# Kernel optimization log

Measured on AMD Instinct MI355X. Metric: run time of the kernel, lower is better.

## Reference

```python
import jax, jax.numpy as jnp
import numpy as np

BS, N, NP, K = 2, 4096, 1024, 8   # batch, fine pts, coarse pts, in-degree per fine node
CI, CO, MID = 32, 16, 32          # in channels (16 skip + 16 interpolated), out channels, radial MLP width
E = BS * N * K


def setup_inputs() -> dict:
    key = jax.random.key(0)
    ks = iter(jax.random.split(key, 64))
    nrm = lambda s, sc=1.0: jax.random.normal(next(ks), s, jnp.float32) * sc
    inp = {}
    inp['h0'] = nrm((BS * N, 16, 1))
    inp['h1'] = nrm((BS * N, 16, 3))
    inp['uph0'] = nrm((BS * NP, 16, 1))
    inp['uph1'] = nrm((BS * NP, 16, 3))
    inp['xyz'] = jax.random.uniform(next(ks), (BS, N, 3), jnp.float32)
    inp['xyz_prev'] = jax.random.uniform(next(ks), (BS, NP, 3), jnp.float32)
    dst = jnp.repeat(jnp.arange(BS * N, dtype=jnp.int32), K)
    src = (dst // N) * N + jax.random.randint(next(ks), (E,), 0, N, jnp.int32)
    inp['edge_src'], inp['edge_dst'] = src, dst
    xf = inp['xyz'].reshape(BS * N, 3)
    inp['r'] = jnp.linalg.norm(xf[src] - xf[dst], axis=-1, keepdims=True)
    # CG basis tensors basis[din,dout]: [E, 2*dout+1, 2*din+1, 2*min(din,dout)+1]
    inp['basis00'] = nrm((E, 1, 1, 1))
    inp['basis01'] = nrm((E, 3, 1, 1))
    inp['basis10'] = nrm((E, 1, 3, 1))
    inp['basis11'] = nrm((E, 3, 3, 3))
    for p, f in (('00', 1), ('01', 1), ('10', 1), ('11', 3)):
        inp['rw1_' + p] = nrm((1, MID), 0.5)
        inp['rb1_' + p] = jnp.zeros((MID,), jnp.float32)
        inp['rw2_' + p] = nrm((MID, MID), 0.2)
        inp['rb2_' + p] = jnp.zeros((MID,), jnp.float32)
        inp['rw3_' + p] = nrm((MID, CO * CI * f), 0.1)
    inp['wself0'] = nrm((CO, CI), 0.1)
    inp['wself1'] = nrm((CO, CI), 0.1)
    inp['gamma0'] = jnp.ones((CO,), jnp.float32)
    inp['beta0'] = jnp.zeros((CO,), jnp.float32)
    inp['gamma1'] = jnp.ones((CO,), jnp.float32)
    inp['beta1'] = jnp.zeros((CO,), jnp.float32)
    return inp


def _radial(r, w1, b1, w2, b2, w3, f):
    x = jax.nn.relu(r @ w1 + b1)
    x = jax.nn.relu(x @ w2 + b2)
    return (x @ w3).reshape(E, CO, CI, f)


def _pair_msg(basis, hsrc, R):
    # basis [E,mo,mi,f], hsrc [E,ci,mi], R [E,co,ci,f] -> msg [E,co,mo]
    # (fused form of per-edge kernel = sum_f R*basis followed by kernel @ src)
    tmp = jnp.einsum('emnf,ein->eimf', basis, hsrc)
    return jnp.einsum('eoif,eimf->eom', R, tmp)


def _gnorm(h, gamma, beta):
    # GNormSE3: norm over m-dim, LayerNorm+ReLU on norms, rescale phase
    n = jnp.sqrt(jnp.sum(h * h, -1) + 1e-12)           # [Nn,co]
    phase = h / n[..., None]
    mu = jnp.mean(n, -1, keepdims=True)
    var = jnp.var(n, -1, keepdims=True)
    t = jax.nn.relu((n - mu) / jnp.sqrt(var + 1e-5) * gamma + beta)
    return t[..., None] * phase


def _fwd(h0, h1, uph0, uph1, xyz, xyz_prev, r, basis00, basis01, basis10, basis11,
         rw1_00, rb1_00, rw2_00, rb2_00, rw3_00,
         rw1_01, rb1_01, rw2_01, rb2_01, rw3_01,
         rw1_10, rb1_10, rw2_10, rb2_10, rw3_10,
         rw1_11, rb1_11, rw2_11, rb2_11, rw3_11,
         wself0, wself1, gamma0, beta0, gamma1, beta1, edge_src, edge_dst):
    # --- three_nn + inverse-squared-distance interpolation of coarse features ---
    d2 = jnp.sum((xyz[:, :, None, :] - xyz_prev[:, None, :, :]) ** 2, -1)  # [B,N,NP]
    negd, idx = jax.lax.top_k(-d2, 3)
    dist = jnp.sqrt(jnp.maximum(-negd, 0.0))
    d2c = jnp.maximum(dist * dist, 1e-10)
    inv = 1.0 / (d2c + 1e-8)
    w = inv / jnp.sum(inv, -1, keepdims=True)          # [B,N,3]

    def interp(uph):
        C, F = uph.shape[1], uph.shape[2]
        fp = uph.reshape(BS, NP, C * F)
        g = jax.vmap(lambda f_, i_: f_[i_])(fp, idx)   # [B,N,3,C*F]
        return jnp.sum(g * w[..., None], 2).reshape(BS * N, C, F)

    h0c = jnp.concatenate([interp(uph0), h0], 1)       # [BN,CI,1]
    h1c = jnp.concatenate([interp(uph1), h1], 1)       # [BN,CI,3]

    # --- GConvSE3: per-edge CG-basis kernels, mean aggregation, self-interaction ---
    hs0, hs1 = h0c[edge_src], h1c[edge_src]
    R00 = _radial(r, rw1_00, rb1_00, rw2_00, rb2_00, rw3_00, 1)
    R01 = _radial(r, rw1_01, rb1_01, rw2_01, rb2_01, rw3_01, 1)
    R10 = _radial(r, rw1_10, rb1_10, rw2_10, rb2_10, rw3_10, 1)
    R11 = _radial(r, rw1_11, rb1_11, rw2_11, rb2_11, rw3_11, 3)
    msg0 = _pair_msg(basis00, hs0, R00) + _pair_msg(basis10, hs1, R10)  # [E,CO,1]
    msg1 = _pair_msg(basis01, hs0, R01) + _pair_msg(basis11, hs1, R11)  # [E,CO,3]
    agg0 = jax.ops.segment_sum(msg0, edge_dst, num_segments=BS * N) / K  # mean (in-degree K)
    agg1 = jax.ops.segment_sum(msg1, edge_dst, num_segments=BS * N) / K
    out0 = agg0 + jnp.einsum('oi,nim->nom', wself0, h0c)
    out1 = agg1 + jnp.einsum('oi,nim->nom', wself1, h1c)

    return _gnorm(out0, gamma0, beta0), _gnorm(out1, gamma1, beta1)


def reference(h0, h1, uph0, uph1, xyz, xyz_prev, r, basis00, basis01, basis10, basis11,
              rw1_00, rb1_00, rw2_00, rb2_00, rw3_00,
              rw1_01, rb1_01, rw2_01, rb2_01, rw3_01,
              rw1_10, rb1_10, rw2_10, rb2_10, rw3_10,
              rw1_11, rb1_11, rw2_11, rb2_11, rw3_11,
              wself0, wself1, gamma0, beta0, gamma1, beta1, edge_src, edge_dst):
    return _fwd(h0, h1, uph0, uph1, xyz, xyz_prev, r, basis00, basis01, basis10, basis11,
                rw1_00, rb1_00, rw2_00, rb2_00, rw3_00,
                rw1_01, rb1_01, rw2_01, rb2_01, rw3_01,
                rw1_10, rb1_10, rw2_10, rb2_10, rw3_10,
                rw1_11, rb1_11, rw2_11, rb2_11, rw3_11,
                wself0, wself1, gamma0, beta0, gamma1, beta1, edge_src, edge_dst)
```

## Files before the change

### kernel.cpp

```cpp
#include <hip/hip_runtime.h>
#include <hip/hip_bf16.h>
#include <math.h>

#define NPP   1024
#define BN    8192
#define NE    65536

typedef __attribute__((ext_vector_type(8))) short bf16x8;
typedef __attribute__((ext_vector_type(4))) float f32x4;

__device__ __forceinline__ short f2bf(float f) {
  __hip_bfloat16 h = __float2bfloat16(f);
  return *reinterpret_cast<short*>(&h);
}
__device__ __forceinline__ float b2f(short h) {
  unsigned u = ((unsigned)(unsigned short)h) << 16;
  return __uint_as_float(u);
}

__device__ __forceinline__ unsigned long long pkkey(float d, int j) {
  return ((unsigned long long)__float_as_uint(d) << 32) | (unsigned int)j;
}

__global__ __launch_bounds__(256) void interp_kernel(
    const float* __restrict__ h0, const float* __restrict__ h1,
    const float* __restrict__ uph0, const float* __restrict__ uph1,
    const float* __restrict__ xyz, const float* __restrict__ xyzp,
    float* __restrict__ h0c, float* __restrict__ h1c)
{
  const int tid  = threadIdx.x;
  const int lane = tid & 63;
  const int wid  = tid >> 6;
  const int fi   = blockIdx.x * 4 + wid;
  const int b    = fi >> 12;

  const float px = xyz[fi*3+0], py = xyz[fi*3+1], pz = xyz[fi*3+2];

  unsigned long long k0 = ~0ull, k1 = ~0ull, k2 = ~0ull;
  const float* cbase = xyzp + (size_t)b*NPP*3;
  #pragma unroll 4
  for (int j = lane; j < NPP; j += 64) {
    const float* cp = cbase + j*3;
    float ax = px - cp[0], ay = py - cp[1], az = pz - cp[2];
    float dd = fmaf(az, az, fmaf(ay, ay, ax*ax));
    unsigned long long kk = pkkey(dd, j);
    if (kk < k0)      { k2 = k1; k1 = k0; k0 = kk; }
    else if (kk < k1) { k2 = k1; k1 = kk; }
    else if (kk < k2) { k2 = kk; }
  }
  #pragma unroll
  for (int off = 1; off < 64; off <<= 1) {
    unsigned long long b0 = __shfl_xor(k0, off);
    unsigned long long b1 = __shfl_xor(k1, off);
    unsigned long long b2 = __shfl_xor(k2, off);
    unsigned long long c0, c1, c2;
    if (k0 <= b0) {
      c0 = k0;
      if (k1 <= b0) { c1 = k1; c2 = (k2 <= b0) ? k2 : b0; }
      else          { c1 = b0; c2 = (k1 <= b1) ? k1 : b1; }
    } else {
      c0 = b0;
      if (b1 <= k0) { c1 = b1; c2 = (b2 <= k0) ? b2 : k0; }
      else          { c1 = k0; c2 = (b1 <= k1) ? b1 : k1; }
    }
    k0 = c0; k1 = c1; k2 = c2;
  }
  const int i0 = (int)(k0 & 0xffffffffu);
  const int i1 = (int)(k1 & 0xffffffffu);
  const int i2 = (int)(k2 & 0xffffffffu);
  const float dd0 = __uint_as_float((unsigned)(k0 >> 32));
  const float dd1 = __uint_as_float((unsigned)(k1 >> 32));
  const float dd2 = __uint_as_float((unsigned)(k2 >> 32));

  float w0, w1v, w2v;
  {
    float s0 = sqrtf(fmaxf(dd0, 0.f));
    float s1 = sqrtf(fmaxf(dd1, 0.f));
    float s2 = sqrtf(fmaxf(dd2, 0.f));
    w0  = 1.f / (fmaxf(s0*s0, 1e-10f) + 1e-8f);
    w1v = 1.f / (fmaxf(s1*s1, 1e-10f) + 1e-8f);
    w2v = 1.f / (fmaxf(s2*s2, 1e-10f) + 1e-8f);
    float wsum = w0 + w1v + w2v;
    w0 /= wsum; w1v /= wsum; w2v /= wsum;
  }

  const float* u0 = uph0 + (size_t)b*NPP*16;
  const float* u1 = uph1 + (size_t)b*NPP*48;
  if (lane < 16) {
    int c = lane;
    h0c[(size_t)fi*32 + c] = w0*u0[i0*16+c] + w1v*u0[i1*16+c] + w2v*u0[i2*16+c];
    h0c[(size_t)fi*32 + 16 + c] = h0[(size_t)fi*16 + c];
  } else {
    int q = lane - 16;
    h1c[(size_t)fi*96 + q] = w0*u1[i0*48+q] + w1v*u1[i1*48+q] + w2v*u1[i2*48+q];
    h1c[(size_t)fi*96 + 48 + q] = h1[(size_t)fi*48 + q];
  }
}

__global__ __launch_bounds__(256) void repack_bf16(
    const float* __restrict__ w00, const float* __restrict__ w01,
    const float* __restrict__ w10, const float* __restrict__ w11,
    const float* __restrict__ w2_00, const float* __restrict__ w2_01,
    const float* __restrict__ w2_10, const float* __restrict__ w2_11,
    unsigned short* __restrict__ B00, unsigned short* __restrict__ B01,
    unsigned short* __restrict__ B10, unsigned short* __restrict__ B11,
    unsigned short* __restrict__ W2H, unsigned short* __restrict__ W2L)
{
  int idx = blockIdx.x * 256 + threadIdx.x;
  if (idx < 49152) {
    int a = idx & 16383;
    int i = a & 31, o = (a >> 5) & 15, k = a >> 9;
    int src = k*512 + o*32 + i;
    if (idx < 16384)      B00[a] = (unsigned short)f2bf(w00[src]);
    else if (idx < 32768) B01[a] = (unsigned short)f2bf(w01[src]);
    else                  B10[a] = (unsigned short)f2bf(w10[src]);
  } else if (idx < 98304) {
    int a = idx - 49152;
    int i = a & 31, o = (a >> 5) & 15, s = a >> 9;
    int f = s >> 5, k = s & 31;
    B11[a] = (unsigned short)f2bf(w11[k*1536 + (o*32+i)*3 + f]);
  } else if (idx < 102400) {
    int a = idx - 98304;
    int p = a >> 10, rem = a & 1023;
    int b = rem >> 5, aa = rem & 31;
    const float* w2p = p==0?w2_00 : p==1?w2_01 : p==2?w2_10 : w2_11;
    W2H[a] = (unsigned short)f2bf(w2p[aa*32 + b]);
  } else if (idx < 106496) {
    int a = idx - 102400;
    int p = a >> 10, rem = a & 1023;
    int b = rem >> 5, aa = rem & 31;
    const float* w2p = p==0?w2_00 : p==1?w2_01 : p==2?w2_10 : w2_11;
    float v = w2p[aa*32 + b];
    short h = f2bf(v);
    W2L[a] = (unsigned short)f2bf(v - b2f(h));
  }
}

struct EP {
  const float *r; const int *esrc;
  const float *b00, *b01, *b10, *b11;
  const float *w1_00, *b1_00, *b2_00;
  const float *w1_01, *b1_01, *b2_01;
  const float *w1_10, *b1_10, *b2_10;
  const float *w1_11, *b1_11, *b2_11;
  const unsigned short *B00, *B01, *B10, *B11, *W2H, *W2L;
  const float *h0c, *h1c;
  float *agg0, *agg1;
};

__global__ __launch_bounds__(256) void edge_mfma(EP P)
{
  __shared__ float x2L[32*260];

  const int tid  = threadIdx.x;
  const int wid  = tid >> 6;
  const int lane = tid & 63;
  const int el   = lane & 15;
  const int kg   = lane >> 4;
  const int kg4  = kg << 2;
  const int eb   = blockIdx.x * 64 + wid * 16;
  const int e    = eb + el;
  const int isl  = kg * 8;

  const int   sidx = P.esrc[e];
  const float rv   = P.r[e];

  const f32x4 zero4 = {0.f, 0.f, 0.f, 0.f};

  #pragma unroll
  for (int p = 0; p < 4; ++p) {
    const float* w1p = p==0?P.w1_00 : p==1?P.w1_01 : p==2?P.w1_10 : P.w1_11;
    const float* b1p = p==0?P.b1_00 : p==1?P.b1_01 : p==2?P.b1_10 : P.b1_11;
    const float* b2p = p==0?P.b2_00 : p==1?P.b2_01 : p==2?P.b2_10 : P.b2_11;
    const unsigned short* w2hp = P.W2H + p*1024;
    const unsigned short* w2lp = P.W2L + p*1024;
    f32x4 wa  = *(const f32x4*)(w1p + isl);
    f32x4 wb  = *(const f32x4*)(w1p + isl + 4);
    f32x4 ba  = *(const f32x4*)(b1p + isl);
    f32x4 bbv = *(const f32x4*)(b1p + isl + 4);
    bf16x8 bh0 = *(const bf16x8*)(w2hp + el*32 + isl);
    bf16x8 bh1 = *(const bf16x8*)(w2hp + (16+el)*32 + isl);
    bf16x8 bl0 = *(const bf16x8*)(w2lp + el*32 + isl);
    bf16x8 bl1 = *(const bf16x8*)(w2lp + (16+el)*32 + isl);
    float b2v0 = b2p[el];
    float b2v1 = b2p[16 + el];
    bf16x8 axh, axl;
    #pragma unroll
    for (int j = 0; j < 4; ++j) {
      float v0 = fmaxf(fmaf(rv, wa[j], ba[j]),  0.f);
      float v1 = fmaxf(fmaf(rv, wb[j], bbv[j]), 0.f);
      short h0s = f2bf(v0), h1s_ = f2bf(v1);
      axh[j]   = h0s;  axl[j]   = f2bf(v0 - b2f(h0s));
      axh[j+4] = h1s_; axl[j+4] = f2bf(v1 - b2f(h1s_));
    }
    f32x4 z0 = __builtin_amdgcn_mfma_f32_16x16x32_bf16(axl, bh0, zero4, 0,0,0);
    z0 = __builtin_amdgcn_mfma_f32_16x16x32_bf16(axh, bl0, z0, 0,0,0);
    z0 = __builtin_amdgcn_mfma_f32_16x16x32_bf16(axh, bh0, z0, 0,0,0);
    f32x4 z1 = __builtin_amdgcn_mfma_f32_16x16x32_bf16(axl, bh1, zero4, 0,0,0);
    z1 = __builtin_amdgcn_mfma_f32_16x16x32_bf16(axh, bl1, z1, 0,0,0);
    z1 = __builtin_amdgcn_mfma_f32_16x16x32_bf16(axh, bh1, z1, 0,0,0);
    f32x4 xv0, xv1;
    #pragma unroll
    for (int j = 0; j < 4; ++j) {
      xv0[j] = fmaxf(z0[j] + b2v0, 0.f);
      xv1[j] = fmaxf(z1[j] + b2v1, 0.f);
    }
    *(f32x4*)&x2L[el*260      + wid*64 + p*16 + kg4] = xv0;
    *(f32x4*)&x2L[(16+el)*260 + wid*64 + p*16 + kg4] = xv1;
  }

  f32x4 h0a = *(const f32x4*)(P.h0c + (size_t)sidx*32 + isl);
  f32x4 h0b = *(const f32x4*)(P.h0c + (size_t)sidx*32 + isl + 4);
  float h1sl[24];
  {
    const float* hp = P.h1c + (size_t)sidx*96 + isl*3;
    #pragma unroll
    for (int q = 0; q < 6; ++q) {
      f32x4 v = *(const f32x4*)(hp + q*4);
      h1sl[q*4+0]=v[0]; h1sl[q*4+1]=v[1]; h1sl[q*4+2]=v[2]; h1sl[q*4+3]=v[3];
    }
  }

  bf16x8 a_h0;
  #pragma unroll
  for (int j = 0; j < 4; ++j) { a_h0[j] = f2bf(h0a[j]); a_h0[j+4] = f2bf(h0b[j]); }

  const int xrow = wid*64 + kg4;

  f32x4 macc0 = zero4;
  {
    const unsigned short* bb = P.B00 + el*32 + isl;
    #pragma unroll 4
    for (int t = 0; t < 32; ++t) {
      bf16x8 bv = *(const bf16x8*)(bb + t*512);
      f32x4 z = __builtin_amdgcn_mfma_f32_16x16x32_bf16(a_h0, bv, zero4, 0, 0, 0);
      f32x4 xs = *(const f32x4*)&x2L[t*260 + xrow + 0];
      macc0[0] = fmaf(xs[0], z[0], macc0[0]);
      macc0[1] = fmaf(xs[1], z[1], macc0[1]);
      macc0[2] = fmaf(xs[2], z[2], macc0[2]);
      macc0[3] = fmaf(xs[3], z[3], macc0[3]);
    }
  }
  {
    f32x4 bv = *(const f32x4*)(P.b00 + eb + kg4);
    macc0[0]*=bv[0]; macc0[1]*=bv[1]; macc0[2]*=bv[2]; macc0[3]*=bv[3];
  }

  {
    const float* bp = P.b10 + (size_t)e*3;
    float c0 = bp[0], c1 = bp[1], c2 = bp[2];
    bf16x8 a_t;
    #pragma unroll
    for (int j = 0; j < 8; ++j)
      a_t[j] = f2bf(c0*h1sl[j*3+0] + c1*h1sl[j*3+1] + c2*h1sl[j*3+2]);
    const unsigned short* bb = P.B10 + el*32 + isl;
    #pragma unroll 4
    for (int t = 0; t < 32; ++t) {
      bf16x8 bv = *(const bf16x8*)(bb + t*512);
      f32x4 z = __builtin_amdgcn_mfma_f32_16x16x32_bf16(a_t, bv, zero4, 0, 0, 0);
      f32x4 xs = *(const f32x4*)&x2L[t*260 + xrow + 32];
      macc0[0] = fmaf(xs[0], z[0], macc0[0]);
      macc0[1] = fmaf(xs[1], z[1], macc0[1]);
      macc0[2] = fmaf(xs[2], z[2], macc0[2]);
      macc0[3] = fmaf(xs[3], z[3], macc0[3]);
    }
  }
  {
    float s = macc0[0]+macc0[1]+macc0[2]+macc0[3];
    s += __shfl_xor(s, 16);
    if ((kg & 1) == 0)
      P.agg0[(size_t)((eb >> 3) + (kg >> 1))*16 + el] = s * 0.125f;
  }

  f32x4 c01 = zero4;
  {
    const unsigned short* bb = P.B01 + el*32 + isl;
    #pragma unroll 4
    for (int t = 0; t < 32; ++t) {
      bf16x8 bv = *(const bf16x8*)(bb + t*512);
      f32x4 z = __builtin_amdgcn_mfma_f32_16x16x32_bf16(a_h0, bv, zero4, 0, 0, 0);
      f32x4 xs = *(const f32x4*)&x2L[t*260 + xrow + 16];
      c01[0] = fmaf(xs[0], z[0], c01[0]);
      c01[1] = fmaf(xs[1], z[1], c01[1]);
      c01[2] = fmaf(xs[2], z[2], c01[2]);
      c01[3] = fmaf(xs[3], z[3], c01[3]);
    }
  }
  f32x4 m1a, m1b, m1c;
  {
    const float* bp = P.b01 + (size_t)(eb + kg4)*3;
    f32x4 q0 = *(const f32x4*)(bp);
    f32x4 q1 = *(const f32x4*)(bp + 4);
    f32x4 q2 = *(const f32x4*)(bp + 8);
    m1a[0]=c01[0]*q0[0]; m1a[1]=c01[1]*q0[3]; m1a[2]=c01[2]*q1[2]; m1a[3]=c01[3]*q2[1];
    m1b[0]=c01[0]*q0[1]; m1b[1]=c01[1]*q1[0]; m1b[2]=c01[2]*q1[3]; m1b[3]=c01[3]*q2[2];
    m1c[0]=c01[0]*q0[2]; m1c[1]=c01[1]*q1[1]; m1c[2]=c01[2]*q2[0]; m1c[3]=c01[3]*q2[3];
  }

  {
    const float* b11e = P.b11 + (size_t)e*27;
    #pragma unroll 1
    for (int f = 0; f < 3; ++f) {
      float bm[9];
      #pragma unroll
      for (int mn = 0; mn < 9; ++mn) bm[mn] = b11e[mn*3 + f];
      bf16x8 am0, am1, am2;
      #pragma unroll
      for (int j = 0; j < 8; ++j) {
        float hn0 = h1sl[j*3+0], hn1 = h1sl[j*3+1], hn2 = h1sl[j*3+2];
        am0[j] = f2bf(bm[0]*hn0 + bm[1]*hn1 + bm[2]*hn2);
        am1[j] = f2bf(bm[3]*hn0 + bm[4]*hn1 + bm[5]*hn2);
        am2[j] = f2bf(bm[6]*hn0 + bm[7]*hn1 + bm[8]*hn2);
      }
      const unsigned short* bb = P.B11 + (size_t)f*16384 + el*32 + isl;
      #pragma unroll 4
      for (int t = 0; t < 32; ++t) {
        bf16x8 bv = *(const bf16x8*)(bb + t*512);
        f32x4 z0 = __builtin_amdgcn_mfma_f32_16x16x32_bf16(am0, bv, zero4, 0, 0, 0);
        f32x4 z1 = __builtin_amdgcn_mfma_f32_16x16x32_bf16(am1, bv, zero4, 0, 0, 0);
        f32x4 z2 = __builtin_amdgcn_mfma_f32_16x16x32_bf16(am2, bv, zero4, 0, 0, 0);
        f32x4 xs = *(const f32x4*)&x2L[t*260 + xrow + 48];
        m1a[0] = fmaf(xs[0], z0[0], m1a[0]);
        m1a[1] = fmaf(xs[1], z0[1], m1a[1]);
        m1a[2] = fmaf(xs[2], z0[2], m1a[2]);
        m1a[3] = fmaf(xs[3], z0[3], m1a[3]);
        m1b[0] = fmaf(xs[0], z1[0], m1b[0]);
        m1b[1] = fmaf(xs[1], z1[1], m1b[1]);
        m1b[2] = fmaf(xs[2], z1[2], m1b[2]);
        m1b[3] = fmaf(xs[3], z1[3], m1b[3]);
        m1c[0] = fmaf(xs[0], z2[0], m1c[0]);
        m1c[1] = fmaf(xs[1], z2[1], m1c[1]);
        m1c[2] = fmaf(xs[2], z2[2], m1c[2]);
        m1c[3] = fmaf(xs[3], z2[3], m1c[3]);
      }
    }
  }

  {
    float sa = m1a[0]+m1a[1]+m1a[2]+m1a[3]; sa += __shfl_xor(sa, 16);
    float sb = m1b[0]+m1b[1]+m1b[2]+m1b[3]; sb += __shfl_xor(sb, 16);
    float sc = m1c[0]+m1c[1]+m1c[2]+m1c[3]; sc += __shfl_xor(sc, 16);
    if ((kg & 1) == 0) {
      float* p = P.agg1 + (size_t)((eb >> 3) + (kg >> 1))*48 + el*3;
      p[0] = sa * 0.125f; p[1] = sb * 0.125f; p[2] = sc * 0.125f;
    }
  }
}

__global__ __launch_bounds__(256) void gnorm_kernel(
    const float* __restrict__ agg0, const float* __restrict__ agg1,
    const float* __restrict__ h0c, const float* __restrict__ h1c,
    const float* __restrict__ ws0, const float* __restrict__ ws1,
    const float* __restrict__ g0, const float* __restrict__ be0,
    const float* __restrict__ g1, const float* __restrict__ be1,
    float* __restrict__ out)
{
  const int gt  = blockIdx.x * 256 + threadIdx.x;
  const int fi  = gt >> 2;
  const int t4  = gt & 3;
  const int ob  = t4 * 4;

  const float* h0p = h0c + (size_t)fi*32;
  const float* h1p = h1c + (size_t)fi*96;

  float o0[4];
  #pragma unroll
  for (int oo = 0; oo < 4; ++oo) {
    int o = ob + oo;
    float a = agg0[(size_t)fi*16 + o];
    #pragma unroll
    for (int i = 0; i < 32; ++i)
      a = fmaf(ws0[o*32+i], h0p[i], a);
    o0[oo] = a;
  }
  {
    float n0[4], lmu = 0.f;
    #pragma unroll
    for (int oo = 0; oo < 4; ++oo) { n0[oo] = sqrtf(fmaf(o0[oo], o0[oo], 1e-12f)); lmu += n0[oo]; }
    lmu += __shfl_xor(lmu, 1); lmu += __shfl_xor(lmu, 2);
    float mu = lmu * 0.0625f;
    float lv = 0.f;
    #pragma unroll
    for (int oo = 0; oo < 4; ++oo) { float d = n0[oo]-mu; lv = fmaf(d, d, lv); }
    lv += __shfl_xor(lv, 1); lv += __shfl_xor(lv, 2);
    float inv = 1.f / sqrtf(lv * 0.0625f + 1e-5f);
    #pragma unroll
    for (int oo = 0; oo < 4; ++oo) {
      int o = ob + oo;
      float t = fmaxf(fmaf((n0[oo]-mu)*inv, g0[o], be0[o]), 0.f);
      out[(size_t)fi*16 + o] = t * (o0[oo] / n0[oo]);
    }
  }

  float o1[12];
  #pragma unroll
  for (int oo = 0; oo < 4; ++oo) {
    int o = ob + oo;
    float a0 = agg1[(size_t)fi*48 + o*3+0];
    float a1 = agg1[(size_t)fi*48 + o*3+1];
    float a2 = agg1[(size_t)fi*48 + o*3+2];
    #pragma unroll
    for (int i = 0; i < 32; ++i) {
      float wv = ws1[o*32+i];
      a0 = fmaf(wv, h1p[i*3+0], a0);
      a1 = fmaf(wv, h1p[i*3+1], a1);
      a2 = fmaf(wv, h1p[i*3+2], a2);
    }
    o1[oo*3+0] = a0; o1[oo*3+1] = a1; o1[oo*3+2] = a2;
  }
  {
    float n1[4], lmu = 0.f;
    #pragma unroll
    for (int oo = 0; oo < 4; ++oo) {
      float s = fmaf(o1[oo*3+0], o1[oo*3+0], 1e-12f);
      s = fmaf(o1[oo*3+1], o1[oo*3+1], s);
      s = fmaf(o1[oo*3+2], o1[oo*3+2], s);
      n1[oo] = sqrtf(s); lmu += n1[oo];
    }
    lmu += __shfl_xor(lmu, 1); lmu += __shfl_xor(lmu, 2);
    float mu = lmu * 0.0625f;
    float lv = 0.f;
    #pragma unroll
    for (int oo = 0; oo < 4; ++oo) { float d = n1[oo]-mu; lv = fmaf(d, d, lv); }
    lv += __shfl_xor(lv, 1); lv += __shfl_xor(lv, 2);
    float inv = 1.f / sqrtf(lv * 0.0625f + 1e-5f);
    float* out1 = out + (size_t)BN*16;
    #pragma unroll
    for (int oo = 0; oo < 4; ++oo) {
      int o = ob + oo;
      float t = fmaxf(fmaf((n1[oo]-mu)*inv, g1[o], be1[o]), 0.f);
      #pragma unroll
      for (int m = 0; m < 3; ++m)
        out1[(size_t)fi*48 + o*3+m] = t * (o1[oo*3+m] / n1[oo]);
    }
  }
}

extern "C" void kernel_launch(void* const* d_in, const int* in_sizes, int n_in,
                              void* d_out, int out_size, void* d_ws, size_t ws_size,
                              hipStream_t stream)
{
  (void)in_sizes; (void)n_in; (void)out_size; (void)ws_size;
  const float* h0   = (const float*)d_in[0];
  const float* h1   = (const float*)d_in[1];
  const float* uph0 = (const float*)d_in[2];
  const float* uph1 = (const float*)d_in[3];
  const float* xyz  = (const float*)d_in[4];
  const float* xyzp = (const float*)d_in[5];
  const int*   esrc = (const int*)d_in[6];
  const float* rr   = (const float*)d_in[8];

  float* wsp  = (float*)d_ws;
  float* h0c  = wsp;
  float* h1c  = h0c + (size_t)BN*32;
  float* agg0 = h1c + (size_t)BN*96;
  float* agg1 = agg0 + (size_t)BN*16;
  unsigned short* B00 = (unsigned short*)(agg1 + (size_t)BN*48);
  unsigned short* B01 = B00 + 16384;
  unsigned short* B10 = B01 + 16384;
  unsigned short* B11 = B10 + 16384;
  unsigned short* W2H = B11 + 49152;
  unsigned short* W2L = W2H + 4096;

  interp_kernel<<<BN/4, 256, 0, stream>>>(h0, h1, uph0, uph1, xyz, xyzp, h0c, h1c);
  repack_bf16<<<416, 256, 0, stream>>>(
      (const float*)d_in[17], (const float*)d_in[22],
      (const float*)d_in[27], (const float*)d_in[32],
      (const float*)d_in[15], (const float*)d_in[20],
      (const float*)d_in[25], (const float*)d_in[30],
      B00, B01, B10, B11, W2H, W2L);

  EP P;
  P.r = rr; P.esrc = esrc;
  P.b00 = (const float*)d_in[9];  P.b01 = (const float*)d_in[10];
  P.b10 = (const float*)d_in[11]; P.b11 = (const float*)d_in[12];
  P.w1_00 = (const float*)d_in[13]; P.b1_00 = (const float*)d_in[14]; P.b2_00 = (const float*)d_in[16];
  P.w1_01 = (const float*)d_in[18]; P.b1_01 = (const float*)d_in[19]; P.b2_01 = (const float*)d_in[21];
  P.w1_10 = (const float*)d_in[23]; P.b1_10 = (const float*)d_in[24]; P.b2_10 = (const float*)d_in[26];
  P.w1_11 = (const float*)d_in[28]; P.b1_11 = (const float*)d_in[29]; P.b2_11 = (const float*)d_in[31];
  P.B00 = B00; P.B01 = B01; P.B10 = B10; P.B11 = B11; P.W2H = W2H; P.W2L = W2L;
  P.h0c = h0c; P.h1c = h1c; P.agg0 = agg0; P.agg1 = agg1;

  edge_mfma<<<NE/64, 256, 0, stream>>>(P);

  gnorm_kernel<<<BN*4/256, 256, 0, stream>>>(agg0, agg1, h0c, h1c,
      (const float*)d_in[33], (const float*)d_in[34],
      (const float*)d_in[35], (const float*)d_in[36],
      (const float*)d_in[37], (const float*)d_in[38],
      (float*)d_out);
}
```

Measured before the change: 105.0 us.

## Process two edge groups per wave to reuse weight loads, store radial features in fp16

Each wave now handles 32 edges as two 16-edge groups, so every bf16 weight fragment loaded from global memory feeds two MFMAs instead of one, halving weight-load traffic per edge. The shared-memory radial hidden activations and the per-edge h1 source features are stored as fp16 to keep LDS and register use down, and launch bounds request 4 blocks per CU. The costs are more register pressure, extra fp16 conversions in the inner loops, and some precision loss in the radial activations.

```diff
diff --git a/kernel.cpp b/kernel.cpp
--- a/kernel.cpp
+++ b/kernel.cpp
@@ -1,5 +1,6 @@
 #include <hip/hip_runtime.h>
 #include <hip/hip_bf16.h>
+#include <hip/hip_fp16.h>
 #include <math.h>
 
 #define NPP   1024
@@ -16,6 +17,14 @@
 __device__ __forceinline__ float b2f(short h) {
   unsigned u = ((unsigned)(unsigned short)h) << 16;
   return __uint_as_float(u);
+}
+__device__ __forceinline__ unsigned short f2h(float f) {
+  __half h = __float2half(f);
+  return *reinterpret_cast<unsigned short*>(&h);
+}
+__device__ __forceinline__ float h2f(unsigned short u) {
+  __half h = *reinterpret_cast<__half*>(&u);
+  return __half2float(h);
 }
 
 __device__ __forceinline__ unsigned long long pkkey(float d, int j) {
@@ -148,9 +157,11 @@
   float *agg0, *agg1;
 };
 
-__global__ __launch_bounds__(256) void edge_mfma(EP P)
+#define LD8(BB, T) (*(const bf16x8*)((BB) + (size_t)(T)*512))
+
+__global__ __launch_bounds__(256, 4) void edge_mfma(EP P)
 {
-  __shared__ float x2L[32*260];
+  __shared__ __align__(16) unsigned short x2Lh[32*520];
 
   const int tid  = threadIdx.x;
   const int wid  = tid >> 6;
@@ -158,14 +169,19 @@
   const int el   = lane & 15;
   const int kg   = lane >> 4;
   const int kg4  = kg << 2;
-  const int eb   = blockIdx.x * 64 + wid * 16;
-  const int e    = eb + el;
   const int isl  = kg * 8;
-
-  const int   sidx = P.esrc[e];
-  const float rv   = P.r[e];
+  const int eb   = blockIdx.x * 128 + wid * 32;
+  const int xb   = wid*128 + kg4;
 
   const f32x4 zero4 = {0.f, 0.f, 0.f, 0.f};
+
+  int   sidx[2];
+  float rv[2];
+  #pragma unroll
+  for (int g = 0; g < 2; ++g) {
+    sidx[g] = P.esrc[eb + g*16 + el];
+    rv[g]   = P.r[eb + g*16 + el];
+  }
 
   #pragma unroll
   for (int p = 0; p < 4; ++p) {
@@ -184,164 +200,169 @@
     bf16x8 bl1 = *(const bf16x8*)(w2lp + (16+el)*32 + isl);
     float b2v0 = b2p[el];
     float b2v1 = b2p[16 + el];
-    bf16x8 axh, axl;
-    #pragma unroll
-    for (int j = 0; j < 4; ++j) {
-      float v0 = fmaxf(fmaf(rv, wa[j], ba[j]),  0.f);
-      float v1 = fmaxf(fmaf(rv, wb[j], bbv[j]), 0.f);
-      short h0s = f2bf(v0), h1s_ = f2bf(v1);
-      axh[j]   = h0s;  axl[j]   = f2bf(v0 - b2f(h0s));
-      axh[j+4] = h1s_; axl[j+4] = f2bf(v1 - b2f(h1s_));
-    }
-    f32x4 z0 = __builtin_amdgcn_mfma_f32_16x16x32_bf16(axl, bh0, zero4, 0,0,0);
-    z0 = __builtin_amdgcn_mfma_f32_16x16x32_bf16(axh, bl0, z0, 0,0,0);
-    z0 = __builtin_amdgcn_mfma_f32_16x16x32_bf16(axh, bh0, z0, 0,0,0);
-    f32x4 z1 = __builtin_amdgcn_mfma_f32_16x16x32_bf16(axl, bh1, zero4, 0,0,0);
-    z1 = __builtin_amdgcn_mfma_f32_16x16x32_bf16(axh, bl1, z1, 0,0,0);
-    z1 = __builtin_amdgcn_mfma_f32_16x16x32_bf16(axh, bh1, z1, 0,0,0);
-    f32x4 xv0, xv1;
-    #pragma unroll
-    for (int j = 0; j < 4; ++j) {
-      xv0[j] = fmaxf(z0[j] + b2v0, 0.f);
-      xv1[j] = fmaxf(z1[j] + b2v1, 0.f);
-    }
-    *(f32x4*)&x2L[el*260      + wid*64 + p*16 + kg4] = xv0;
-    *(f32x4*)&x2L[(16+el)*260 + wid*64 + p*16 + kg4] = xv1;
-  }
-
-  f32x4 h0a = *(const f32x4*)(P.h0c + (size_t)sidx*32 + isl);
-  f32x4 h0b = *(const f32x4*)(P.h0c + (size_t)sidx*32 + isl + 4);
-  float h1sl[24];
-  {
-    const float* hp = P.h1c + (size_t)sidx*96 + isl*3;
+    #pragma unroll
+    for (int g = 0; g < 2; ++g) {
+      bf16x8 axh, axl;
+      #pragma unroll
+      for (int j = 0; j < 4; ++j) {
+        float v0 = fmaxf(fmaf(rv[g], wa[j], ba[j]),  0.f);
+        float v1 = fmaxf(fmaf(rv[g], wb[j], bbv[j]), 0.f);
+        short h0s = f2bf(v0), h1s_ = f2bf(v1);
+        axh[j]   = h0s;  axl[j]   = f2bf(v0 - b2f(h0s));
+        axh[j+4] = h1s_; axl[j+4] = f2bf(v1 - b2f(h1s_));
+      }
+      f32x4 z0 = __builtin_amdgcn_mfma_f32_16x16x32_bf16(axl, bh0, zero4, 0,0,0);
+      z0 = __builtin_amdgcn_mfma_f32_16x16x32_bf16(axh, bl0, z0, 0,0,0);
+      z0 = __builtin_amdgcn_mfma_f32_16x16x32_bf16(axh, bh0, z0, 0,0,0);
+      f32x4 z1 = __builtin_amdgcn_mfma_f32_16x16x32_bf16(axl, bh1, zero4, 0,0,0);
+      z1 = __builtin_amdgcn_mfma_f32_16x16x32_bf16(axh, bl1, z1, 0,0,0);
+      z1 = __builtin_amdgcn_mfma_f32_16x16x32_bf16(axh, bh1, z1, 0,0,0);
+      ushort4 o0, o1v;
+      o0.x  = f2h(fmaxf(z0[0] + b2v0, 0.f));
+      o0.y  = f2h(fmaxf(z0[1] + b2v0, 0.f));
+      o0.z  = f2h(fmaxf(z0[2] + b2v0, 0.f));
+      o0.w  = f2h(fmaxf(z0[3] + b2v0, 0.f));
+      o1v.x = f2h(fmaxf(z1[0] + b2v1, 0.f));
+      o1v.y = f2h(fmaxf(z1[1] + b2v1, 0.f));
+      o1v.z = f2h(fmaxf(z1[2] + b2v1, 0.f));
+      o1v.w = f2h(fmaxf(z1[3] + b2v1, 0.f));
+      *(ushort4*)&x2Lh[el*520      + wid*128 + g*64 + p*16 + kg4] = o0;
+      *(ushort4*)&x2Lh[(16+el)*520 + wid*128 + g*64 + p*16 + kg4] = o1v;
+    }
+  }
+
+  bf16x8 a_h0[2];
+  unsigned int h1p[2][12];
+  #pragma unroll
+  for (int g = 0; g < 2; ++g) {
+    f32x4 ha = *(const f32x4*)(P.h0c + (size_t)sidx[g]*32 + isl);
+    f32x4 hb = *(const f32x4*)(P.h0c + (size_t)sidx[g]*32 + isl + 4);
+    #pragma unroll
+    for (int j = 0; j < 4; ++j) { a_h0[g][j] = f2bf(ha[j]); a_h0[g][j+4] = f2bf(hb[j]); }
+    const float* hp = P.h1c + (size_t)sidx[g]*96 + isl*3;
     #pragma unroll
     for (int q = 0; q < 6; ++q) {
       f32x4 v = *(const f32x4*)(hp + q*4);
-      h1sl[q*4+0]=v[0]; h1sl[q*4+1]=v[1]; h1sl[q*4+2]=v[2]; h1sl[q*4+3]=v[3];
-    }
-  }
-
-  bf16x8 a_h0;
-  #pragma unroll
-  for (int j = 0; j < 4; ++j) { a_h0[j] = f2bf(h0a[j]); a_h0[j+4] = f2bf(h0b[j]); }
-
-  const int xrow = wid*64 + kg4;
-
-  f32x4 macc0 = zero4;
-  {
-    const unsigned short* bb = P.B00 + el*32 + isl;
-    #pragma unroll 4
-    for (int t = 0; t < 32; ++t) {
-      bf16x8 bv = *(const bf16x8*)(bb + t*512);
-      f32x4 z = __builtin_amdgcn_mfma_f32_16x16x32_bf16(a_h0, bv, zero4, 0, 0, 0);
-      f32x4 xs = *(const f32x4*)&x2L[t*260 + xrow + 0];
-      macc0[0] = fmaf(xs[0], z[0], macc0[0]);
-      macc0[1] = fmaf(xs[1], z[1], macc0[1]);
-      macc0[2] = fmaf(xs[2], z[2], macc0[2]);
-      macc0[3] = fmaf(xs[3], z[3], macc0[3]);
-    }
-  }
-  {
-    f32x4 bv = *(const f32x4*)(P.b00 + eb + kg4);
-    macc0[0]*=bv[0]; macc0[1]*=bv[1]; macc0[2]*=bv[2]; macc0[3]*=bv[3];
-  }
-
-  {
-    const float* bp = P.b10 + (size_t)e*3;
-    float c0 = bp[0], c1 = bp[1], c2 = bp[2];
-    bf16x8 a_t;
-    #pragma unroll
-    for (int j = 0; j < 8; ++j)
-      a_t[j] = f2bf(c0*h1sl[j*3+0] + c1*h1sl[j*3+1] + c2*h1sl[j*3+2]);
-    const unsigned short* bb = P.B10 + el*32 + isl;
-    #pragma unroll 4
-    for (int t = 0; t < 32; ++t) {
-      bf16x8 bv = *(const bf16x8*)(bb + t*512);
-      f32x4 z = __builtin_amdgcn_mfma_f32_16x16x32_bf16(a_t, bv, zero4, 0, 0, 0);
-      f32x4 xs = *(const f32x4*)&x2L[t*260 + xrow + 32];
-      macc0[0] = fmaf(xs[0], z[0], macc0[0]);
-      macc0[1] = fmaf(xs[1], z[1], macc0[1]);
-      macc0[2] = fmaf(xs[2], z[2], macc0[2]);
-      macc0[3] = fmaf(xs[3], z[3], macc0[3]);
-    }
-  }
-  {
-    float s = macc0[0]+macc0[1]+macc0[2]+macc0[3];
-    s += __shfl_xor(s, 16);
-    if ((kg & 1) == 0)
-      P.agg0[(size_t)((eb >> 3) + (kg >> 1))*16 + el] = s * 0.125f;
-  }
-
-  f32x4 c01 = zero4;
-  {
-    const unsigned short* bb = P.B01 + el*32 + isl;
-    #pragma unroll 4
-    for (int t = 0; t < 32; ++t) {
-      bf16x8 bv = *(const bf16x8*)(bb + t*512);
-      f32x4 z = __builtin_amdgcn_mfma_f32_16x16x32_bf16(a_h0, bv, zero4, 0, 0, 0);
-      f32x4 xs = *(const f32x4*)&x2L[t*260 + xrow + 16];
-      c01[0] = fmaf(xs[0], z[0], c01[0]);
-      c01[1] = fmaf(xs[1], z[1], c01[1]);
-      c01[2] = fmaf(xs[2], z[2], c01[2]);
-      c01[3] = fmaf(xs[3], z[3], c01[3]);
-    }
-  }
-  f32x4 m1a, m1b, m1c;
-  {
-    const float* bp = P.b01 + (size_t)(eb + kg4)*3;
+      h1p[g][q*2]   = (unsigned)f2h(v[0]) | ((unsigned)f2h(v[1]) << 16);
+      h1p[g][q*2+1] = (unsigned)f2h(v[2]) | ((unsigned)f2h(v[3]) << 16);
+    }
+  }
+#define HG(G, I) h2f((unsigned short)(((I) & 1) ? (h1p[G][(I)>>1] >> 16) : (h1p[G][(I)>>1] & 0xffffu)))
+
+#define CVT4(PTR) ({ ushort4 u_ = *(const ushort4*)(PTR); \
+    f32x4 r_; r_[0]=h2f(u_.x); r_[1]=h2f(u_.y); r_[2]=h2f(u_.z); r_[3]=h2f(u_.w); r_; })
+
+#define F1_LOOP2(BPTR, POFF, A0, A1, ACC0, ACC1)                              \
+  { const unsigned short* bb_ = (BPTR) + el*32 + isl;                         \
+    _Pragma("unroll 4")                                                       \
+    for (int t = 0; t < 32; ++t) {                                            \
+      bf16x8 bv_ = LD8(bb_, t);                                               \
+      f32x4 z0_ = __builtin_amdgcn_mfma_f32_16x16x32_bf16((A0), bv_, zero4, 0,0,0); \
+      f32x4 z1_ = __builtin_amdgcn_mfma_f32_16x16x32_bf16((A1), bv_, zero4, 0,0,0); \
+      f32x4 xs0_ = CVT4(&x2Lh[t*520 + xb + (POFF)]);                          \
+      f32x4 xs1_ = CVT4(&x2Lh[t*520 + xb + 64 + (POFF)]);                     \
+      ACC0[0] = fmaf(xs0_[0], z0_[0], ACC0[0]);                               \
+      ACC0[1] = fmaf(xs0_[1], z0_[1], ACC0[1]);                               \
+      ACC0[2] = fmaf(xs0_[2], z0_[2], ACC0[2]);                               \
+      ACC0[3] = fmaf(xs0_[3], z0_[3], ACC0[3]);                               \
+      ACC1[0] = fmaf(xs1_[0], z1_[0], ACC1[0]);                               \
+      ACC1[1] = fmaf(xs1_[1], z1_[1], ACC1[1]);                               \
+      ACC1[2] = fmaf(xs1_[2], z1_[2], ACC1[2]);                               \
+      ACC1[3] = fmaf(xs1_[3], z1_[3], ACC1[3]); } }
+
+  f32x4 macc0[2]; macc0[0] = zero4; macc0[1] = zero4;
+  F1_LOOP2(P.B00, 0, a_h0[0], a_h0[1], macc0[0], macc0[1]);
+  #pragma unroll
+  for (int g = 0; g < 2; ++g) {
+    f32x4 bv = *(const f32x4*)(P.b00 + eb + g*16 + kg4);
+    macc0[g][0]*=bv[0]; macc0[g][1]*=bv[1]; macc0[g][2]*=bv[2]; macc0[g][3]*=bv[3];
+  }
+
+  f32x4 c01[2]; c01[0] = zero4; c01[1] = zero4;
+  F1_LOOP2(P.B01, 16, a_h0[0], a_h0[1], c01[0], c01[1]);
+  f32x4 m1[2][3];
+  #pragma unroll
+  for (int g = 0; g < 2; ++g) {
+    const float* bp = P.b01 + (size_t)(eb + g*16 + kg4)*3;
     f32x4 q0 = *(const f32x4*)(bp);
     f32x4 q1 = *(const f32x4*)(bp + 4);
     f32x4 q2 = *(const f32x4*)(bp + 8);
-    m1a[0]=c01[0]*q0[0]; m1a[1]=c01[1]*q0[3]; m1a[2]=c01[2]*q1[2]; m1a[3]=c01[3]*q2[1];
-    m1b[0]=c01[0]*q0[1]; m1b[1]=c01[1]*q1[0]; m1b[2]=c01[2]*q1[3]; m1b[3]=c01[3]*q2[2];
-    m1c[0]=c01[0]*q0[2]; m1c[1]=c01[1]*q1[1]; m1c[2]=c01[2]*q2[0]; m1c[3]=c01[3]*q2[3];
+    m1[g][0][0]=c01[g][0]*q0[0]; m1[g][0][1]=c01[g][1]*q0[3]; m1[g][0][2]=c01[g][2]*q1[2]; m1[g][0][3]=c01[g][3]*q2[1];
+    m1[g][1][0]=c01[g][0]*q0[1]; m1[g][1][1]=c01[g][1]*q1[0]; m1[g][1][2]=c01[g][2]*q1[3]; m1[g][1][3]=c01[g][3]*q2[2];
+    m1[g][2][0]=c01[g][0]*q0[2]; m1[g][2][1]=c01[g][1]*q1[1]; m1[g][2][2]=c01[g][2]*q2[0]; m1[g][2][3]=c01[g][3]*q2[3];
   }
 
   {
-    const float* b11e = P.b11 + (size_t)e*27;
-    #pragma unroll 1
-    for (int f = 0; f < 3; ++f) {
+    bf16x8 a_t[2];
+    #pragma unroll
+    for (int g = 0; g < 2; ++g) {
+      const float* bp = P.b10 + (size_t)(eb + g*16 + el)*3;
+      float c0 = bp[0], c1 = bp[1], c2 = bp[2];
+      #pragma unroll
+      for (int j = 0; j < 8; ++j)
+        a_t[g][j] = f2bf(c0*HG(g, j*3+0) + c1*HG(g, j*3+1) + c2*HG(g, j*3+2));
+    }
+    F1_LOOP2(P.B10, 32, a_t[0], a_t[1], macc0[0], macc0[1]);
+  }
+
+  #pragma unroll
+  for (int g = 0; g < 2; ++g) {
+    float s = macc0[g][0]+macc0[g][1]+macc0[g][2]+macc0[g][3];
+    s += __shfl_xor(s, 16);
+    if ((kg & 1) == 0)
+      P.agg0[(size_t)((eb >> 3) + g*2 + (kg >> 1))*16 + el] = s * 0.125f;
+  }
+
+  #pragma unroll 1
+  for (int f = 0; f < 3; ++f) {
+    bf16x8 am[2][3];
+    #pragma unroll
+    for (int g = 0; g < 2; ++g) {
+      const float* b11e = P.b11 + (size_t)(eb + g*16 + el)*27;
       float bm[9];
       #pragma unroll
       for (int mn = 0; mn < 9; ++mn) bm[mn] = b11e[mn*3 + f];
-      bf16x8 am0, am1, am2;
       #pragma unroll
       for (int j = 0; j < 8; ++j) {
-        float hn0 = h1sl[j*3+0], hn1 = h1sl[j*3+1], hn2 = h1sl[j*3+2];
-        am0[j] = f2bf(bm[0]*hn0 + bm[1]*hn1 + bm[2]*hn2);
-        am1[j] = f2bf(bm[3]*hn0 + bm[4]*hn1 + bm[5]*hn2);
-        am2[j] = f2bf(bm[6]*hn0 + bm[7]*hn1 + bm[8]*hn2);
+        float hn0 = HG(g, j*3+0), hn1 = HG(g, j*3+1), hn2 = HG(g, j*3+2);
+        am[g][0][j] = f2bf(bm[0]*hn0 + bm[1]*hn1 + bm[2]*hn2);
+        am[g][1][j] = f2bf(bm[3]*hn0 + bm[4]*hn1 + bm[5]*hn2);
+        am[g][2][j] = f2bf(bm[6]*hn0 + bm[7]*hn1 + bm[8]*hn2);
       }
-      const unsigned short* bb = P.B11 + (size_t)f*16384 + el*32 + isl;
-      #pragma unroll 4
-      for (int t = 0; t < 32; ++t) {
-        bf16x8 bv = *(const bf16x8*)(bb + t*512);
-        f32x4 z0 = __builtin_amdgcn_mfma_f32_16x16x32_bf16(am0, bv, zero4, 0, 0, 0);
-        f32x4 z1 = __builtin_amdgcn_mfma_f32_16x16x32_bf16(am1, bv, zero4, 0, 0, 0);
-        f32x4 z2 = __builtin_amdgcn_mfma_f32_16x16x32_bf16(am2, bv, zero4, 0, 0, 0);
-        f32x4 xs = *(const f32x4*)&x2L[t*260 + xrow + 48];
-        m1a[0] = fmaf(xs[0], z0[0], m1a[0]);
-        m1a[1] = fmaf(xs[1], z0[1], m1a[1]);
-        m1a[2] = fmaf(xs[2], z0[2], m1a[2]);
-        m1a[3] = fmaf(xs[3], z0[3], m1a[3]);
-        m1b[0] = fmaf(xs[0], z1[0], m1b[0]);
-        m1b[1] = fmaf(xs[1], z1[1], m1b[1]);
-        m1b[2] = fmaf(xs[2], z1[2], m1b[2]);
-        m1b[3] = fmaf(xs[3], z1[3], m1b[3]);
-        m1c[0] = fmaf(xs[0], z2[0], m1c[0]);
-        m1c[1] = fmaf(xs[1], z2[1], m1c[1]);
-        m1c[2] = fmaf(xs[2], z2[2], m1c[2]);
-        m1c[3] = fmaf(xs[3], z2[3], m1c[3]);
+    }
+    const unsigned short* bb = P.B11 + (size_t)f*16384 + el*32 + isl;
+    #pragma unroll 4
+    for (int t = 0; t < 32; ++t) {
+      bf16x8 bv = LD8(bb, t);
+      #pragma unroll
+      for (int g = 0; g < 2; ++g) {
+        f32x4 z0 = __builtin_amdgcn_mfma_f32_16x16x32_bf16(am[g][0], bv, zero4, 0, 0, 0);
+        f32x4 z1 = __builtin_amdgcn_mfma_f32_16x16x32_bf16(am[g][1], bv, zero4, 0, 0, 0);
+        f32x4 z2 = __builtin_amdgcn_mfma_f32_16x16x32_bf16(am[g][2], bv, zero4, 0, 0, 0);
+        f32x4 xs = CVT4(&x2Lh[t*520 + xb + g*64 + 48]);
+        m1[g][0][0] = fmaf(xs[0], z0[0], m1[g][0][0]);
+        m1[g][0][1] = fmaf(xs[1], z0[1], m1[g][0][1]);
+        m1[g][0][2] = fmaf(xs[2], z0[2], m1[g][0][2]);
+        m1[g][0][3] = fmaf(xs[3], z0[3], m1[g][0][3]);
+        m1[g][1][0] = fmaf(xs[0], z1[0], m1[g][1][0]);
+        m1[g][1][1] = fmaf(xs[1], z1[1], m1[g][1][1]);
+        m1[g][1][2] = fmaf(xs[2], z1[2], m1[g][1][2]);
+        m1[g][1][3] = fmaf(xs[3], z1[3], m1[g][1][3]);
+        m1[g][2][0] = fmaf(xs[0], z2[0], m1[g][2][0]);
+        m1[g][2][1] = fmaf(xs[1], z2[1], m1[g][2][1]);
+        m1[g][2][2] = fmaf(xs[2], z2[2], m1[g][2][2]);
+        m1[g][2][3] = fmaf(xs[3], z2[3], m1[g][2][3]);
       }
     }
   }
 
-  {
-    float sa = m1a[0]+m1a[1]+m1a[2]+m1a[3]; sa += __shfl_xor(sa, 16);
-    float sb = m1b[0]+m1b[1]+m1b[2]+m1b[3]; sb += __shfl_xor(sb, 16);
-    float sc = m1c[0]+m1c[1]+m1c[2]+m1c[3]; sc += __shfl_xor(sc, 16);
+  #pragma unroll
+  for (int g = 0; g < 2; ++g) {
+    float sa = m1[g][0][0]+m1[g][0][1]+m1[g][0][2]+m1[g][0][3]; sa += __shfl_xor(sa, 16);
+    float sb = m1[g][1][0]+m1[g][1][1]+m1[g][1][2]+m1[g][1][3]; sb += __shfl_xor(sb, 16);
+    float sc = m1[g][2][0]+m1[g][2][1]+m1[g][2][2]+m1[g][2][3]; sc += __shfl_xor(sc, 16);
     if ((kg & 1) == 0) {
-      float* p = P.agg1 + (size_t)((eb >> 3) + (kg >> 1))*48 + el*3;
+      float* p = P.agg1 + (size_t)((eb >> 3) + g*2 + (kg >> 1))*48 + el*3;
       p[0] = sa * 0.125f; p[1] = sb * 0.125f; p[2] = sc * 0.125f;
     }
   }
@@ -481,7 +502,7 @@
   P.B00 = B00; P.B01 = B01; P.B10 = B10; P.B11 = B11; P.W2H = W2H; P.W2L = W2L;
   P.h0c = h0c; P.h1c = h1c; P.agg0 = agg0; P.agg1 = agg1;
 
-  edge_mfma<<<NE/64, 256, 0, stream>>>(P);
+  edge_mfma<<<NE/128, 256, 0, stream>>>(P);
 
   gnorm_kernel<<<BN*4/256, 256, 0, stream>>>(agg0, agg1, h0c, h1c,
       (const float*)d_in[33], (const float*)d_in[34],
```

After: 123.0 us. 17.1% more time.
